# Optimization experiments

Hardware: AMD Instinct MI355X
Metric: run time of the kernel (lower is better)

The kernel has to match this reference:

```python
import jax, jax.numpy as jnp
import numpy as np

N, X_DIM, Y_DIM, HID = 1024, 128, 128, 256


def setup_inputs() -> dict:
    key = jax.random.key(0)
    k1, k2, k3, k4 = jax.random.split(key, 4)
    return {
        "x_samples": jax.random.normal(k1, (N, X_DIM), dtype=jnp.float32),
        "y_samples": jax.random.normal(k2, (N, Y_DIM), dtype=jnp.float32),
        "W1": jax.random.normal(k3, (X_DIM + Y_DIM, HID), dtype=jnp.float32) * 0.05,
        "b1": jnp.zeros((HID,), dtype=jnp.float32),
        "W2": jax.random.normal(k4, (HID, 1), dtype=jnp.float32) * 0.05,
        "b2": jnp.zeros((1,), dtype=jnp.float32),
    }


def reference(x_samples, y_samples, W1, b1, W2, b2):
    n = y_samples.shape[0]
    x_dim = x_samples.shape[-1]
    # Split first linear so we never materialize the N^2 concat:
    W1x, W1y = W1[:x_dim], W1[x_dim:]
    pre_x = x_samples @ W1x  # [N, H]
    pre_y = y_samples @ W1y  # [N, H]
    # T0: F on matched pairs (x_i, y_i)
    T0 = jax.nn.relu(pre_x + pre_y + b1) @ W2 + b2  # [N, 1]
    # T1[i, j] = F([x_j, y_i]) - 1.0  (all-pairs grid)
    h = jax.nn.relu(pre_x[None, :, :] + pre_y[:, None, :] + b1)  # [N, N, H]
    T1 = h @ W2 + b2 - 1.0  # [N, N, 1]
    lse = jax.nn.logsumexp(T1, axis=1)  # [N, 1]
    lower_bound = T0.mean() - jnp.exp(lse - jnp.log(jnp.float32(n))).mean()
    return lower_bound
```

## Files before the change

kernel.cpp:

```cpp
#include <hip/hip_runtime.h>

typedef _Float16 h2 __attribute__((ext_vector_type(2)));
typedef unsigned int u32;

#define OFF_XP   0u
#define OFF_YP   0x40000u
#define OFF_W1XP 0x80000u
#define OFF_W1YP 0x90000u
#define OFF_A2   0x100000u
#define OFF_C2   0x180000u

__device__ __forceinline__ u32 pack2(float a, float b) {
  h2 v; v.x = (_Float16)a; v.y = (_Float16)b;
  return __builtin_bit_cast(u32, v);
}
__device__ __forceinline__ h2 as_h2(u32 u) { return __builtin_bit_cast(h2, u); }

__device__ __forceinline__ float fdot2(h2 a, h2 b, float c) {
#if __has_builtin(__builtin_amdgcn_fdot2)
  return __builtin_amdgcn_fdot2(a, b, c, false);
#else
  return (float)a.x * (float)b.x + (float)a.y * (float)b.y + c;
#endif
}
__device__ __forceinline__ h2 relu2(h2 t) {
  h2 z; z.x = (_Float16)0.0f; z.y = (_Float16)0.0f;
  return __builtin_elementwise_max(t, z);
}

__global__ void k0_pack(const float* __restrict__ x, const float* __restrict__ y,
                        const float* __restrict__ W1, u32* __restrict__ wsu,
                        float* __restrict__ out) {
  const int b = blockIdx.x, tid = threadIdx.x;
  if (b == 0 && tid == 0) out[0] = 0.0f;
  if (b < 128) {
    const float* src = (b < 64) ? x : y;
    u32* dst = wsu + ((b < 64) ? (OFF_XP >> 2) : (OFF_YP >> 2));
    const int bb = b & 63, kt = bb & 3, rt = bb >> 2;
    __shared__ float sT[64][33];
    const int kl = tid & 31, rg = tid >> 5;
#pragma unroll
    for (int p = 0; p < 8; ++p) {
      const int r = p * 8 + rg;
      sT[r][kl] = src[(rt * 64 + r) * 128 + kt * 32 + kl];
    }
    __syncthreads();
    const int rl = tid & 63, kg = tid >> 6;
#pragma unroll
    for (int q = 0; q < 4; ++q) {
      const int kkl = q * 4 + kg;
      dst[(kt * 16 + kkl) * 1024 + rt * 64 + rl] =
          pack2(sT[rl][2 * kkl], sT[rl][2 * kkl + 1]);
    }
  } else {
    const int kk = b - 128, h = tid;
    wsu[(OFF_W1XP >> 2) + kk * 256 + h] =
        pack2(W1[(2 * kk) * 256 + h], W1[(2 * kk + 1) * 256 + h]);
    wsu[(OFF_W1YP >> 2) + kk * 256 + h] =
        pack2(W1[(128 + 2 * kk) * 256 + h], W1[(129 + 2 * kk) * 256 + h]);
  }
}

__global__ __launch_bounds__(256) void k1_pre(u32* __restrict__ wsu,
                                              const float* __restrict__ b1) {
  const int b = blockIdx.x, tid = threadIdx.x;
  const int mat = b >> 8;
  const int bb = b & 255, ht = bb & 7, rt = bb >> 3;
  const int tx = tid & 31, ty = tid >> 5;
  const int h0 = ht * 32 + ty * 4;
  const u32* xp  = wsu + (mat ? (OFF_YP >> 2) : (OFF_XP >> 2)) + rt * 32 + tx;
  const u32* w1p = wsu + (mat ? (OFF_W1YP >> 2) : (OFF_W1XP >> 2)) + h0;
  u32* dst = wsu + (mat ? (OFF_C2 >> 2) : (OFF_A2 >> 2)) + rt * 4096 + tx * 128;

  float acc[4];
  if (mat) {
    const float4 bv = *(const float4*)(b1 + h0);
    acc[0] = bv.x; acc[1] = bv.y; acc[2] = bv.z; acc[3] = bv.w;
  } else {
    acc[0] = acc[1] = acc[2] = acc[3] = 0.0f;
  }

  u32 XR[8]; uint4 WR[8];
#pragma unroll
  for (int s = 0; s < 8; ++s) {
    XR[s] = xp[s * 1024];
    WR[s] = *(const uint4*)(w1p + s * 256);
  }
#pragma unroll 8
  for (int kk = 0; kk < 56; ++kk) {
    const int s = kk & 7;
    const h2 xr = as_h2(XR[s]); const uint4 wv = WR[s];
    XR[s] = xp[(kk + 8) * 1024];
    WR[s] = *(const uint4*)(w1p + (kk + 8) * 256);
    acc[0] = fdot2(xr, as_h2(wv.x), acc[0]);
    acc[1] = fdot2(xr, as_h2(wv.y), acc[1]);
    acc[2] = fdot2(xr, as_h2(wv.z), acc[2]);
    acc[3] = fdot2(xr, as_h2(wv.w), acc[3]);
  }
#pragma unroll
  for (int kk = 56; kk < 64; ++kk) {
    const int s = kk & 7;
    const h2 xr = as_h2(XR[s]); const uint4 wv = WR[s];
    acc[0] = fdot2(xr, as_h2(wv.x), acc[0]);
    acc[1] = fdot2(xr, as_h2(wv.y), acc[1]);
    acc[2] = fdot2(xr, as_h2(wv.z), acc[2]);
    acc[3] = fdot2(xr, as_h2(wv.w), acc[3]);
  }
  const int hh0 = ht * 16 + ty * 2;
  uint2 sv;
  sv.x = pack2(acc[0], acc[1]);
  sv.y = pack2(acc[2], acc[3]);
  *(uint2*)(dst + hh0) = sv;
}

__global__ __launch_bounds__(256) void k2_main(const u32* __restrict__ wsu,
                                               const float* __restrict__ W2g,
                                               const float* __restrict__ B2,
                                               float* __restrict__ out) {
  const int bi = blockIdx.x >> 5, bj = blockIdx.x & 31;
  const int tid = threadIdx.x;
  const int tx = tid & 15, ty = tid >> 4;

  __shared__ uint4 sA4[32 * 32];
  __shared__ uint4 sC4[32 * 32];
  __shared__ uint4 sW4[32];
  __shared__ float sred[4];
  u32* sW2 = (u32*)sW4;

  {
    const u32* gA = wsu + (OFF_A2 >> 2) + bj * 4096;
    const u32* gC = wsu + (OFF_C2 >> 2) + bi * 4096;
    const int j = tid >> 3, q8 = tid & 7, sw = (j >> 1) & 7;
#pragma unroll
    for (int m = 0; m < 4; ++m) {
      const int q = q8 + 8 * m;
      sA4[j * 32 + (q ^ sw)] = *(const uint4*)(gA + j * 128 + q * 4);
      sC4[j * 32 + (q ^ sw)] = *(const uint4*)(gC + j * 128 + q * 4);
    }
    if (tid < 128) sW2[tid] = pack2(W2g[2 * tid], W2g[2 * tid + 1]);
  }
  __syncthreads();

  const uint4* rA0 = sA4 + (2 * tx) * 32;
  const uint4* rA1 = rA0 + 32;
  const uint4* rC0 = sC4 + (2 * ty) * 32;
  const uint4* rC1 = rC0 + 32;
  const int swzA = tx & 7, swzC = ty & 7;

  float acc[4] = {0.0f, 0.0f, 0.0f, 0.0f};
#pragma unroll 4
  for (int g = 0; g < 32; ++g) {
    const uint4 av0 = rA0[g ^ swzA], av1 = rA1[g ^ swzA];
    const uint4 cv0 = rC0[g ^ swzC], cv1 = rC1[g ^ swzC];
    const uint4 wv = sW4[g];
    const u32 a0[4] = {av0.x, av0.y, av0.z, av0.w};
    const u32 a1[4] = {av1.x, av1.y, av1.z, av1.w};
    const u32 c0[4] = {cv0.x, cv0.y, cv0.z, cv0.w};
    const u32 c1[4] = {cv1.x, cv1.y, cv1.z, cv1.w};
    const u32 ww[4] = {wv.x, wv.y, wv.z, wv.w};
#pragma unroll
    for (int m = 0; m < 4; ++m) {
      const h2 A0 = as_h2(a0[m]), A1 = as_h2(a1[m]);
      const h2 C0 = as_h2(c0[m]), C1 = as_h2(c1[m]);
      const h2 w = as_h2(ww[m]);
      acc[0] = fdot2(relu2(A0 + C0), w, acc[0]);
      acc[1] = fdot2(relu2(A1 + C0), w, acc[1]);
      acc[2] = fdot2(relu2(A0 + C1), w, acc[2]);
      acc[3] = fdot2(relu2(A1 + C1), w, acc[3]);
    }
  }

  const float b2 = B2[0];
  float val = 0.0f;
#pragma unroll
  for (int p = 0; p < 4; ++p) val += __expf(acc[p] + (b2 - 1.0f));
  val *= -1.0f / 1048576.0f;
  if (bi == bj && tx == ty)
    val += (acc[0] + acc[3] + 2.0f * b2) * (1.0f / 1024.0f);
#pragma unroll
  for (int off = 32; off > 0; off >>= 1) val += __shfl_down(val, off, 64);
  if ((tid & 63) == 0) sred[tid >> 6] = val;
  __syncthreads();
  if (tid == 0) atomicAdd(out, sred[0] + sred[1] + sred[2] + sred[3]);
}

extern "C" void kernel_launch(void* const* d_in, const int* in_sizes, int n_in,
                              void* d_out, int out_size, void* d_ws, size_t ws_size,
                              hipStream_t stream) {
  const float* x  = (const float*)d_in[0];
  const float* y  = (const float*)d_in[1];
  const float* W1 = (const float*)d_in[2];
  const float* b1 = (const float*)d_in[3];
  const float* W2 = (const float*)d_in[4];
  const float* b2 = (const float*)d_in[5];
  u32* wsu = (u32*)d_ws;

  hipLaunchKernelGGL(k0_pack, dim3(192), dim3(256), 0, stream, x, y, W1, wsu,
                     (float*)d_out);
  hipLaunchKernelGGL(k1_pre, dim3(512), dim3(256), 0, stream, wsu, b1);
  hipLaunchKernelGGL(k2_main, dim3(1024), dim3(256), 0, stream, wsu, W2, b2,
                     (float*)d_out);
}
```

Baseline: 91.52 us.

## Enlarge main kernel tile to 64x64 with 4x4 register blocking

The all-pairs kernel now gives each block a 64x64 tile and each thread a 4x4 output micro-tile instead of 2x2. This raises reuse of the A and C values loaded from shared memory, and the shared-memory reads are double-buffered in registers one step ahead. W2 is pre-packed to fp16 once in the pack kernel and read straight from global memory instead of being staged in LDS by every block. The trade-offs are more registers and LDS per block and only 256 blocks, which lowers occupancy and may leave CUs underused.

Measured after the change: 133.5 us. 1.46x slower.

```diff
diff --git a/kernel.cpp b/kernel.cpp
--- a/kernel.cpp
+++ b/kernel.cpp
@@ -7,6 +7,7 @@
 #define OFF_YP   0x40000u
 #define OFF_W1XP 0x80000u
 #define OFF_W1YP 0x90000u
+#define OFF_W2H  0xA0000u
 #define OFF_A2   0x100000u
 #define OFF_C2   0x180000u
 
@@ -29,11 +30,14 @@
 }
 
 __global__ void k0_pack(const float* __restrict__ x, const float* __restrict__ y,
-                        const float* __restrict__ W1, u32* __restrict__ wsu,
-                        float* __restrict__ out) {
+                        const float* __restrict__ W1, const float* __restrict__ W2,
+                        u32* __restrict__ wsu, float* __restrict__ out) {
   const int b = blockIdx.x, tid = threadIdx.x;
-  if (b == 0 && tid == 0) out[0] = 0.0f;
   if (b < 128) {
+    if (b == 0) {
+      if (tid == 0) out[0] = 0.0f;
+      if (tid < 128) wsu[(OFF_W2H >> 2) + tid] = pack2(W2[2 * tid], W2[2 * tid + 1]);
+    }
     const float* src = (b < 64) ? x : y;
     u32* dst = wsu + ((b < 64) ? (OFF_XP >> 2) : (OFF_YP >> 2));
     const int bb = b & 63, kt = bb & 3, rt = bb >> 2;
@@ -114,69 +118,90 @@
 }
 
 __global__ __launch_bounds__(256) void k2_main(const u32* __restrict__ wsu,
-                                               const float* __restrict__ W2g,
                                                const float* __restrict__ B2,
                                                float* __restrict__ out) {
-  const int bi = blockIdx.x >> 5, bj = blockIdx.x & 31;
+  const int bi = blockIdx.x >> 4, bj = blockIdx.x & 15;
   const int tid = threadIdx.x;
   const int tx = tid & 15, ty = tid >> 4;
 
-  __shared__ uint4 sA4[32 * 32];
-  __shared__ uint4 sC4[32 * 32];
-  __shared__ uint4 sW4[32];
+  __shared__ uint4 sA4[64 * 32];
+  __shared__ uint4 sC4[64 * 32];
   __shared__ float sred[4];
-  u32* sW2 = (u32*)sW4;
 
   {
-    const u32* gA = wsu + (OFF_A2 >> 2) + bj * 4096;
-    const u32* gC = wsu + (OFF_C2 >> 2) + bi * 4096;
-    const int j = tid >> 3, q8 = tid & 7, sw = (j >> 1) & 7;
-#pragma unroll
-    for (int m = 0; m < 4; ++m) {
-      const int q = q8 + 8 * m;
+    const u32* gA = wsu + (OFF_A2 >> 2) + bj * 8192;
+    const u32* gC = wsu + (OFF_C2 >> 2) + bi * 8192;
+    const int j = tid >> 2, t4 = tid & 3, sw = (j >> 2) & 7;
+#pragma unroll
+    for (int m = 0; m < 8; ++m) {
+      const int q = t4 + 4 * m;
       sA4[j * 32 + (q ^ sw)] = *(const uint4*)(gA + j * 128 + q * 4);
       sC4[j * 32 + (q ^ sw)] = *(const uint4*)(gC + j * 128 + q * 4);
     }
-    if (tid < 128) sW2[tid] = pack2(W2g[2 * tid], W2g[2 * tid + 1]);
   }
   __syncthreads();
 
-  const uint4* rA0 = sA4 + (2 * tx) * 32;
-  const uint4* rA1 = rA0 + 32;
-  const uint4* rC0 = sC4 + (2 * ty) * 32;
-  const uint4* rC1 = rC0 + 32;
+  const uint4* pA = sA4 + (tx * 4) * 32;
+  const uint4* pC = sC4 + (ty * 4) * 32;
+  const uint4* pW = (const uint4*)(wsu + (OFF_W2H >> 2));
   const int swzA = tx & 7, swzC = ty & 7;
 
-  float acc[4] = {0.0f, 0.0f, 0.0f, 0.0f};
+  float acc[16];
+#pragma unroll
+  for (int p = 0; p < 16; ++p) acc[p] = 0.0f;
+
+  uint4 Ar[2][4], Cr[2][4];
+#pragma unroll
+  for (int r = 0; r < 4; ++r) {
+    Ar[0][r] = pA[r * 32 + swzA];
+    Cr[0][r] = pC[r * 32 + swzC];
+  }
 #pragma unroll 4
   for (int g = 0; g < 32; ++g) {
-    const uint4 av0 = rA0[g ^ swzA], av1 = rA1[g ^ swzA];
-    const uint4 cv0 = rC0[g ^ swzC], cv1 = rC1[g ^ swzC];
-    const uint4 wv = sW4[g];
-    const u32 a0[4] = {av0.x, av0.y, av0.z, av0.w};
-    const u32 a1[4] = {av1.x, av1.y, av1.z, av1.w};
-    const u32 c0[4] = {cv0.x, cv0.y, cv0.z, cv0.w};
-    const u32 c1[4] = {cv1.x, cv1.y, cv1.z, cv1.w};
+    const int s = g & 1, ns = s ^ 1;
+    if (g < 31) {
+      const int g1 = g + 1;
+#pragma unroll
+      for (int r = 0; r < 4; ++r) {
+        Ar[ns][r] = pA[r * 32 + (g1 ^ swzA)];
+        Cr[ns][r] = pC[r * 32 + (g1 ^ swzC)];
+      }
+    }
+    const uint4 wv = pW[g];
     const u32 ww[4] = {wv.x, wv.y, wv.z, wv.w};
+    u32 aa[4][4], cc[4][4];
+#pragma unroll
+    for (int r = 0; r < 4; ++r) {
+      aa[r][0] = Ar[s][r].x; aa[r][1] = Ar[s][r].y;
+      aa[r][2] = Ar[s][r].z; aa[r][3] = Ar[s][r].w;
+      cc[r][0] = Cr[s][r].x; cc[r][1] = Cr[s][r].y;
+      cc[r][2] = Cr[s][r].z; cc[r][3] = Cr[s][r].w;
+    }
 #pragma unroll
     for (int m = 0; m < 4; ++m) {
-      const h2 A0 = as_h2(a0[m]), A1 = as_h2(a1[m]);
-      const h2 C0 = as_h2(c0[m]), C1 = as_h2(c1[m]);
       const h2 w = as_h2(ww[m]);
-      acc[0] = fdot2(relu2(A0 + C0), w, acc[0]);
-      acc[1] = fdot2(relu2(A1 + C0), w, acc[1]);
-      acc[2] = fdot2(relu2(A0 + C1), w, acc[2]);
-      acc[3] = fdot2(relu2(A1 + C1), w, acc[3]);
+#pragma unroll
+      for (int ii = 0; ii < 4; ++ii) {
+        const h2 ci = as_h2(cc[ii][m]);
+#pragma unroll
+        for (int jj = 0; jj < 4; ++jj) {
+          acc[ii * 4 + jj] = fdot2(relu2(as_h2(aa[jj][m]) + ci), w, acc[ii * 4 + jj]);
+        }
+      }
     }
   }
 
   const float b2 = B2[0];
   float val = 0.0f;
 #pragma unroll
-  for (int p = 0; p < 4; ++p) val += __expf(acc[p] + (b2 - 1.0f));
+  for (int p = 0; p < 16; ++p) val += __expf(acc[p] + (b2 - 1.0f));
   val *= -1.0f / 1048576.0f;
-  if (bi == bj && tx == ty)
-    val += (acc[0] + acc[3] + 2.0f * b2) * (1.0f / 1024.0f);
+  if (bi == bj && tx == ty) {
+    float d = 0.0f;
+#pragma unroll
+    for (int c = 0; c < 4; ++c) d += acc[c * 5];
+    val += (d + 4.0f * b2) * (1.0f / 1024.0f);
+  }
 #pragma unroll
   for (int off = 32; off > 0; off >>= 1) val += __shfl_down(val, off, 64);
   if ((tid & 63) == 0) sred[tid >> 6] = val;
@@ -195,9 +220,9 @@
   const float* b2 = (const float*)d_in[5];
   u32* wsu = (u32*)d_ws;
 
-  hipLaunchKernelGGL(k0_pack, dim3(192), dim3(256), 0, stream, x, y, W1, wsu,
+  hipLaunchKernelGGL(k0_pack, dim3(192), dim3(256), 0, stream, x, y, W1, W2, wsu,
                      (float*)d_out);
   hipLaunchKernelGGL(k1_pre, dim3(512), dim3(256), 0, stream, wsu, b1);
-  hipLaunchKernelGGL(k2_main, dim3(1024), dim3(256), 0, stream, wsu, W2, b2,
+  hipLaunchKernelGGL(k2_main, dim3(256), dim3(256), 0, stream, wsu, b2,
                      (float*)d_out);
 }
```
